# Optimization experiments

Hardware: AMD Instinct MI355X
Metric: run time of the kernel (lower is better)

Reference implementation:

```python
import jax, jax.numpy as jnp
import numpy as np

D = 128
LN_EPS = 1e-5

def _mlp2(x, W1, b1, W2, b2):
    return jax.nn.silu(x @ W1 + b1) @ W2 + b2

def setup_inputs() -> dict:
    key = jax.random.key(0)
    ks = jax.random.split(key, 20)
    B, N = 2, 512
    inp = {
        'scalar_features': jax.random.normal(ks[0], (B, N, D), jnp.float32),
        'vector_features': jax.random.normal(ks[1], (B, N, 3), jnp.float32),
        'positions': jax.random.normal(ks[2], (B, N, 3), jnp.float32),
        'pair_mask': jnp.ones((B, N, N), jnp.float32),
        'conservation': jax.random.uniform(ks[3], (B, N, 1), jnp.float32),
    }
    s = 0.02
    inp['eW1'] = jax.random.normal(ks[4], (2 * D + 4, D), jnp.float32) * s
    inp['eb1'] = jnp.zeros((D,), jnp.float32)
    inp['eW2'] = jax.random.normal(ks[5], (D, D), jnp.float32) * s
    inp['eb2'] = jnp.zeros((D,), jnp.float32)
    inp['sW1'] = jax.random.normal(ks[6], (2 * D, D), jnp.float32) * s
    inp['sb1'] = jnp.zeros((D,), jnp.float32)
    inp['sW2'] = jax.random.normal(ks[7], (D, D), jnp.float32) * s
    inp['sb2'] = jnp.zeros((D,), jnp.float32)
    inp['vW1'] = jax.random.normal(ks[8], (D, D), jnp.float32) * s
    inp['vb1'] = jnp.zeros((D,), jnp.float32)
    inp['vW2'] = jax.random.normal(ks[9], (D, 1), jnp.float32) * s
    inp['vb2'] = jnp.zeros((1,), jnp.float32)
    inp['ln_w'] = jnp.ones((D,), jnp.float32)
    inp['ln_b'] = jnp.zeros((D,), jnp.float32)
    return inp

def reference(scalar_features, vector_features, positions, pair_mask, conservation,
              eW1, eb1, eW2, eb2, sW1, sb1, sW2, sb2, vW1, vb1, vW2, vb2, ln_w, ln_b):
    N = scalar_features.shape[-2]
    # rel[b,i,j] = pos[b,i] - pos[b,j]
    rel = positions[..., :, None, :] - positions[..., None, :, :]          # [B,N,N,3]
    dist = jnp.maximum(jnp.linalg.norm(rel, axis=-1, keepdims=True), 1e-8)  # [B,N,N,1]
    direction = rel / dist
    feat_i = jnp.broadcast_to(scalar_features[..., :, None, :], scalar_features.shape[:-2] + (N, N, D))
    feat_j = jnp.broadcast_to(scalar_features[..., None, :, :], scalar_features.shape[:-2] + (N, N, D))
    cons_i = jnp.broadcast_to(conservation[..., :, None, :], conservation.shape[:-2] + (N, N, 1))
    cons_j = jnp.broadcast_to(conservation[..., None, :, :], conservation.shape[:-2] + (N, N, 1))
    edge_input = jnp.concatenate([feat_i, feat_j, dist, cons_i, cons_j, pair_mask[..., None]], axis=-1)
    edge_hidden = _mlp2(edge_input, eW1, eb1, eW2, eb2)                    # [B,N,N,D]
    edge_weights = jax.nn.sigmoid(edge_hidden.mean(axis=-1)) * pair_mask   # [B,N,N]
    message_scalar = (edge_hidden * edge_weights[..., None]).sum(axis=-2)  # sum over j -> [B,N,D]
    upd = _mlp2(jnp.concatenate([scalar_features, message_scalar], axis=-1), sW1, sb1, sW2, sb2)
    x = scalar_features + upd
    mu = x.mean(axis=-1, keepdims=True)
    var = x.var(axis=-1, keepdims=True)
    scalar_out = (x - mu) * jax.lax.rsqrt(var + LN_EPS) * ln_w + ln_b
    vector_gate = _mlp2(edge_hidden, vW1, vb1, vW2, vb2)[..., 0] * edge_weights  # [B,N,N]
    vector_message = (vector_gate[..., None] * direction).sum(axis=-2)           # [B,N,3]
    vector_out = vector_features + vector_message
    return scalar_out, vector_out, edge_weights
```

## Files before the change

kernel.cpp:

```cpp
#include <hip/hip_runtime.h>

#define DD 128
#define NN 512
#define NODES 1024

typedef short bf16x8 __attribute__((ext_vector_type(8)));
typedef float f32x4 __attribute__((ext_vector_type(4)));

__device__ __forceinline__ float sigmoidf_(float x) {
  return __builtin_amdgcn_rcpf(1.f + __expf(-x));
}
__device__ __forceinline__ float siluf_(float x) { return x * sigmoidf_(x); }

__device__ __forceinline__ unsigned short f2bf_(float v) {
  unsigned int u = __float_as_uint(v);
  u += 0x7fffu + ((u >> 16) & 1u);
  return (unsigned short)(u >> 16);
}
__device__ __forceinline__ unsigned cvtpk_(float lo, float hi) {
  unsigned r;
  asm("v_cvt_pk_bf16_f32 %0, %1, %2" : "=v"(r) : "v"(lo), "v"(hi));
  return r;
}
__device__ __forceinline__ float bflo_(unsigned u) { return __uint_as_float(u << 16); }
__device__ __forceinline__ float bfhi_(unsigned u) { return __uint_as_float(u & 0xffff0000u); }

__global__ __launch_bounds__(128) void prep_kernel(
    const float* __restrict__ sf, const float* __restrict__ cons,
    const float* __restrict__ eW1, const float* __restrict__ eb1,
    const float* __restrict__ eW2, const float* __restrict__ eb2,
    const float* __restrict__ vW1, const float* __restrict__ vb1,
    float* __restrict__ Ag, float* __restrict__ Bvg,
    unsigned short* __restrict__ E2V1T, float* __restrict__ m2,
    float* __restrict__ c1, float* __restrict__ mb)
{
  const int bid = blockIdx.x;
  const int d = threadIdx.x;
  if (bid < NODES) {
    float c = cons[bid];
    float aacc = c * eW1[258*DD + d];
    float bacc = eb1[d] + c * eW1[257*DD + d];
    const float* sfrow = sf + bid*DD;
    #pragma unroll 4
    for (int k = 0; k < DD; ++k) {
      float s = sfrow[k];
      aacc = fmaf(s, eW1[(128+k)*DD + d], aacc);
      bacc = fmaf(s, eW1[k*DD + d], bacc);
    }
    Ag[bid*DD + d]  = aacc;
    Bvg[bid*DD + d] = bacc;
  } else if (bid < NODES + 128) {
    const int k = bid - NODES;
    float acc = 0.f;
    #pragma unroll 4
    for (int t = 0; t < DD; ++t) acc = fmaf(eW2[k*DD + t], vW1[t*DD + d], acc);
    E2V1T[d*DD + (k ^ ((d & 7) << 3))] = f2bf_(acc);
    if (d == 0) {
      float s = 0.f;
      for (int t = 0; t < DD; ++t) s += eW2[k*DD + t];
      m2[k] = s * (1.0f/128.0f);
    }
  } else {
    float acc = vb1[d];
    #pragma unroll 4
    for (int k = 0; k < DD; ++k) acc = fmaf(eb2[k], vW1[k*DD + d], acc);
    c1[d] = acc;
    if (d == 0) {
      float s = 0.f;
      for (int k = 0; k < DD; ++k) s += eb2[k];
      mb[0] = s * (1.0f/128.0f);
    }
  }
}

__global__ __launch_bounds__(256, 2) void edge_kernel(
    const float* __restrict__ sf, const float* __restrict__ vf,
    const float* __restrict__ pos, const float* __restrict__ pm,
    const float* __restrict__ eW1,
    const float* __restrict__ eW2, const float* __restrict__ eb2,
    const float* __restrict__ sW1, const float* __restrict__ sb1,
    const float* __restrict__ sW2, const float* __restrict__ sb2,
    const float* __restrict__ vW2g, const float* __restrict__ vb2g,
    const float* __restrict__ lnw, const float* __restrict__ lnb,
    const float* __restrict__ Ag, const float* __restrict__ Bvg,
    const unsigned short* __restrict__ E2V1Tg, const float* __restrict__ m2g,
    const float* __restrict__ c1g, const float* __restrict__ mbg,
    float* __restrict__ sout, float* __restrict__ vout, float* __restrict__ ewout)
{
  __shared__ __align__(16) unsigned short eTs[128*128];
  __shared__ __align__(16) float BvL[DD], w256L[DD], w259L[DD], m2L[DD];
  __shared__ __align__(16) float c1L[DD], vw2L[DD];
  __shared__ float redS[4], redVx[4], redVy[4], redVz[4], redA[2], redB[2];

  const int tid = threadIdx.x;
  const int ni  = blockIdx.x;
  const int nb  = ni & ~(NN - 1);

  const int l   = tid & 63, w = tid >> 6;
  const int l15 = l & 15,  lg = l >> 4;
  const int d   = tid & 127, sub = tid >> 7;
  const int d0base = lg*8;

  {
    const uint4* src = (const uint4*)E2V1Tg;
    uint4* dst = (uint4*)eTs;
    #pragma unroll
    for (int it = 0; it < 8; ++it) dst[tid + it*256] = src[tid + it*256];
  }
  if (tid < 128) {
    BvL[tid]   = Bvg[(size_t)ni*DD + tid];
    w256L[tid] = eW1[256*DD + tid];
    w259L[tid] = eW1[259*DD + tid];
    m2L[tid]   = m2g[tid];
    c1L[tid]   = c1g[tid];
    vw2L[tid]  = vW2g[tid];
  }
  const float pix = pos[ni*3+0], piy = pos[ni*3+1], piz = pos[ni*3+2];
  const float mbv = mbg[0], vb2v = vb2g[0];

  float Sreg[4][8];
  #pragma unroll
  for (int kk = 0; kk < 4; ++kk)
    #pragma unroll
    for (int m = 0; m < 8; ++m) Sreg[kk][m] = 0.f;
  float vmx = 0.f, vmy = 0.f, vmz = 0.f, swacc = 0.f;

  __syncthreads();

  for (int t = 0; t < 8; ++t) {
    const int row = t*64 + w*16 + l15;
    float px = pos[(nb + row)*3 + 0];
    float py = pos[(nb + row)*3 + 1];
    float pz = pos[(nb + row)*3 + 2];
    float rx = pix - px, ry = piy - py, rz = piz - pz;
    float dist = fmaxf(sqrtf(rx*rx + ry*ry + rz*rz), 1e-8f);
    float inv = __builtin_amdgcn_rcpf(dist);
    float dirx = rx*inv, diry = ry*inv, dirz = rz*inv;
    float mj = pm[(size_t)ni*NN + row];

    uint4 pk0, pk1, pk2, pk3;
    float dot = 0.f;
    const float* agrow = Ag + (size_t)(nb + row)*DD;

#define A_STEP(KK, PK) {                                                        \
    const int d0 = (KK)*32 + d0base;                                            \
    float4 a0 = *(const float4*)(agrow + d0), a1 = *(const float4*)(agrow + d0 + 4); \
    float4 b0 = *(const float4*)&BvL[d0],   b1 = *(const float4*)&BvL[d0+4];    \
    float4 wa0= *(const float4*)&w256L[d0], wa1= *(const float4*)&w256L[d0+4];  \
    float4 wb0= *(const float4*)&w259L[d0], wb1= *(const float4*)&w259L[d0+4];  \
    float4 m20= *(const float4*)&m2L[d0],   m21= *(const float4*)&m2L[d0+4];    \
    float h0 = siluf_(b0.x + a0.x + dist*wa0.x + mj*wb0.x);                     \
    float h1 = siluf_(b0.y + a0.y + dist*wa0.y + mj*wb0.y);                     \
    float h2 = siluf_(b0.z + a0.z + dist*wa0.z + mj*wb0.z);                     \
    float h3 = siluf_(b0.w + a0.w + dist*wa0.w + mj*wb0.w);                     \
    float h4 = siluf_(b1.x + a1.x + dist*wa1.x + mj*wb1.x);                     \
    float h5 = siluf_(b1.y + a1.y + dist*wa1.y + mj*wb1.y);                     \
    float h6 = siluf_(b1.z + a1.z + dist*wa1.z + mj*wb1.z);                     \
    float h7 = siluf_(b1.w + a1.w + dist*wa1.w + mj*wb1.w);                     \
    PK.x = cvtpk_(h0, h1); PK.y = cvtpk_(h2, h3);                               \
    PK.z = cvtpk_(h4, h5); PK.w = cvtpk_(h6, h7);                               \
    dot += h0*m20.x + h1*m20.y + h2*m20.z + h3*m20.w                            \
         + h4*m21.x + h5*m21.y + h6*m21.z + h7*m21.w; }

    A_STEP(0, pk0)
    A_STEP(1, pk1)
    A_STEP(2, pk2)
    A_STEP(3, pk3)
#undef A_STEP

    dot += __shfl_xor(dot, 16);
    dot += __shfl_xor(dot, 32);
    const float w_full = mj * sigmoidf_(dot + mbv);
    if (lg == 0) {
      ewout[(size_t)ni*NN + row] = w_full;
      swacc += w_full;
    }

#define S_STEP(KK, PK) {                                          \
    Sreg[KK][0] = fmaf(w_full, bflo_(PK.x), Sreg[KK][0]);         \
    Sreg[KK][1] = fmaf(w_full, bfhi_(PK.x), Sreg[KK][1]);         \
    Sreg[KK][2] = fmaf(w_full, bflo_(PK.y), Sreg[KK][2]);         \
    Sreg[KK][3] = fmaf(w_full, bfhi_(PK.y), Sreg[KK][3]);         \
    Sreg[KK][4] = fmaf(w_full, bflo_(PK.z), Sreg[KK][4]);         \
    Sreg[KK][5] = fmaf(w_full, bfhi_(PK.z), Sreg[KK][5]);         \
    Sreg[KK][6] = fmaf(w_full, bflo_(PK.w), Sreg[KK][6]);         \
    Sreg[KK][7] = fmaf(w_full, bfhi_(PK.w), Sreg[KK][7]); }

    S_STEP(0, pk0)
    S_STEP(1, pk1)
    S_STEP(2, pk2)
    S_STEP(3, pk3)
#undef S_STEP

    const bf16x8 af0 = __builtin_bit_cast(bf16x8, pk0);
    const bf16x8 af1 = __builtin_bit_cast(bf16x8, pk1);
    const bf16x8 af2 = __builtin_bit_cast(bf16x8, pk2);
    const bf16x8 af3 = __builtin_bit_cast(bf16x8, pk3);

    float gp[4] = {0.f, 0.f, 0.f, 0.f};
    #pragma unroll
    for (int ct = 0; ct < 8; ++ct) {
      const int col = ct*16 + l15;
      const int swz = (col & 7) << 3;
      const unsigned short* ecol = &eTs[col*DD];
      bf16x8 bf0 = *(const bf16x8*)&ecol[(  0 + d0base) ^ swz];
      bf16x8 bf1 = *(const bf16x8*)&ecol[( 32 + d0base) ^ swz];
      bf16x8 bf2 = *(const bf16x8*)&ecol[( 64 + d0base) ^ swz];
      bf16x8 bf3 = *(const bf16x8*)&ecol[( 96 + d0base) ^ swz];
      f32x4 c = {0.f, 0.f, 0.f, 0.f};
      c = __builtin_amdgcn_mfma_f32_16x16x32_bf16(af0, bf0, c, 0, 0, 0);
      c = __builtin_amdgcn_mfma_f32_16x16x32_bf16(af1, bf1, c, 0, 0, 0);
      c = __builtin_amdgcn_mfma_f32_16x16x32_bf16(af2, bf2, c, 0, 0, 0);
      c = __builtin_amdgcn_mfma_f32_16x16x32_bf16(af3, bf3, c, 0, 0, 0);
      const float c1c = c1L[col], vw2c = vw2L[col];
      gp[0] += siluf_(c[0] + c1c) * vw2c;
      gp[1] += siluf_(c[1] + c1c) * vw2c;
      gp[2] += siluf_(c[2] + c1c) * vw2c;
      gp[3] += siluf_(c[3] + c1c) * vw2c;
    }
    #pragma unroll
    for (int r = 0; r < 4; ++r) {
      float v = gp[r];
      v += __shfl_xor(v, 1);
      v += __shfl_xor(v, 2);
      v += __shfl_xor(v, 4);
      v += __shfl_xor(v, 8);
      const int srow = lg*4 + r;
      float wrow = __shfl(w_full, srow);
      float g = (v + vb2v) * wrow;
      float dx = __shfl(dirx, srow);
      float dy = __shfl(diry, srow);
      float dz = __shfl(dirz, srow);
      if (l15 == 0) {
        vmx = fmaf(g, dx, vmx);
        vmy = fmaf(g, dy, vmy);
        vmz = fmaf(g, dz, vmz);
      }
    }
  }

  __syncthreads();
  float* scr   = (float*)eTs;
  float* Spart = scr;
  float* SL    = scr + 512;
  float* partA = scr + 640;
  float* msgL  = scr + 768;
  float* u1L   = scr + 896;
  float* xoL   = scr + 1024;

  #pragma unroll
  for (int kk = 0; kk < 4; ++kk)
    #pragma unroll
    for (int m = 0; m < 8; ++m) {
      float v = Sreg[kk][m];
      v += __shfl_xor(v, 1);
      v += __shfl_xor(v, 2);
      v += __shfl_xor(v, 4);
      v += __shfl_xor(v, 8);
      Sreg[kk][m] = v;
    }
  if (l15 == 0) {
    #pragma unroll
    for (int kk = 0; kk < 4; ++kk)
      #pragma unroll
      for (int m = 0; m < 8; ++m)
        Spart[w*128 + kk*32 + lg*8 + m] = Sreg[kk][m];
  }
  {
    float sw = swacc;
    #pragma unroll
    for (int off = 1; off < 64; off <<= 1) sw += __shfl_xor(sw, off);
    if (l == 0) redS[w] = sw;
  }
  {
    float vx = vmx, vy = vmy, vz = vmz;
    #pragma unroll
    for (int off = 1; off < 64; off <<= 1) {
      vx += __shfl_xor(vx, off);
      vy += __shfl_xor(vy, off);
      vz += __shfl_xor(vz, off);
    }
    if (l == 0) { redVx[w] = vx; redVy[w] = vy; redVz[w] = vz; }
  }
  __syncthreads();
  if (tid < 128) SL[tid] = Spart[tid] + Spart[128+tid] + Spart[256+tid] + Spart[384+tid];
  if (tid == 0) {
    vout[ni*3 + 0] = vf[ni*3 + 0] + redVx[0]+redVx[1]+redVx[2]+redVx[3];
    vout[ni*3 + 1] = vf[ni*3 + 1] + redVy[0]+redVy[1]+redVy[2]+redVy[3];
    vout[ni*3 + 2] = vf[ni*3 + 2] + redVz[0]+redVz[1]+redVz[2]+redVz[3];
  }
  __syncthreads();
  const float sumwv = redS[0] + redS[1] + redS[2] + redS[3];

  float p = 0.f;
  { int k0 = sub*64;
    #pragma unroll 4
    for (int k = k0; k < k0 + 64; ++k) p = fmaf(SL[k], eW2[k*DD + d], p); }
  if (sub) partA[d] = p;
  __syncthreads();
  if (!sub) msgL[d] = p + partA[d] + sumwv * eb2[d];
  __syncthreads();

  float q = 0.f;
  if (!sub) {
    const float* xr = sf + (size_t)ni*DD;
    #pragma unroll 4
    for (int tt = 0; tt < 128; ++tt) q = fmaf(xr[tt], sW1[tt*DD + d], q);
  } else {
    #pragma unroll 4
    for (int tt = 0; tt < 128; ++tt) q = fmaf(msgL[tt], sW1[(128 + tt)*DD + d], q);
  }
  if (sub) partA[d] = q;
  __syncthreads();
  if (!sub) u1L[d] = siluf_(q + partA[d] + sb1[d]);
  __syncthreads();

  float r2 = 0.f;
  { int t0 = sub*64;
    #pragma unroll 4
    for (int tt = t0; tt < t0 + 64; ++tt) r2 = fmaf(u1L[tt], sW2[tt*DD + d], r2); }
  if (sub) partA[d] = r2;
  __syncthreads();
  if (!sub) xoL[d] = sf[(size_t)ni*DD + d] + r2 + partA[d] + sb2[d];
  __syncthreads();

  if (tid < 128) {
    float v = xoL[tid];
    float s1 = v, s2 = v*v;
    #pragma unroll
    for (int off = 1; off < 64; off <<= 1) { s1 += __shfl_xor(s1, off); s2 += __shfl_xor(s2, off); }
    if ((tid & 63) == 0) { redA[tid >> 6] = s1; redB[tid >> 6] = s2; }
  }
  __syncthreads();
  if (tid < 128) {
    float s1 = redA[0] + redA[1], s2 = redB[0] + redB[1];
    float mu = s1 * 0.0078125f;
    float var = s2 * 0.0078125f - mu*mu;
    sout[(size_t)ni*DD + tid] = (xoL[tid] - mu) * rsqrtf(var + 1e-5f) * lnw[tid] + lnb[tid];
  }
}

extern "C" void kernel_launch(void* const* d_in, const int* in_sizes, int n_in,
                              void* d_out, int out_size, void* d_ws, size_t ws_size,
                              hipStream_t stream) {
  const float* sf   = (const float*)d_in[0];
  const float* vf   = (const float*)d_in[1];
  const float* pos  = (const float*)d_in[2];
  const float* pm   = (const float*)d_in[3];
  const float* cons = (const float*)d_in[4];
  const float* eW1  = (const float*)d_in[5];
  const float* eb1  = (const float*)d_in[6];
  const float* eW2  = (const float*)d_in[7];
  const float* eb2  = (const float*)d_in[8];
  const float* sW1  = (const float*)d_in[9];
  const float* sb1  = (const float*)d_in[10];
  const float* sW2  = (const float*)d_in[11];
  const float* sb2  = (const float*)d_in[12];
  const float* vW1  = (const float*)d_in[13];
  const float* vb1  = (const float*)d_in[14];
  const float* vW2  = (const float*)d_in[15];
  const float* vb2  = (const float*)d_in[16];
  const float* lnw  = (const float*)d_in[17];
  const float* lnb  = (const float*)d_in[18];

  float* ws   = (float*)d_ws;
  float* Ag   = ws;
  float* Bvg  = ws + 131072;
  float* m2   = ws + 262144;
  float* c1   = ws + 262272;
  float* mb   = ws + 262400;
  unsigned short* E2V1T = (unsigned short*)(ws + 262404);

  float* sout  = (float*)d_out;
  float* vout  = sout + 131072;
  float* ewout = sout + 134144;

  hipLaunchKernelGGL(prep_kernel, dim3(NODES + 129), dim3(128), 0, stream,
                     sf, cons, eW1, eb1, eW2, eb2, vW1, vb1,
                     Ag, Bvg, E2V1T, m2, c1, mb);
  hipLaunchKernelGGL(edge_kernel, dim3(NODES), dim3(256), 0, stream,
                     sf, vf, pos, pm, eW1, eW2, eb2, sW1, sb1, sW2, sb2,
                     vW2, vb2, lnw, lnb, Ag, Bvg, E2V1T, m2, c1, mb,
                     sout, vout, ewout);
}
```

Measured before the change: 103.5 us.

## Read fused weight matrix from global/L2 instead of staging in LDS, raise occupancy

```diff
diff --git a/kernel.cpp b/kernel.cpp
--- a/kernel.cpp
+++ b/kernel.cpp
@@ -54,7 +54,7 @@
     float acc = 0.f;
     #pragma unroll 4
     for (int t = 0; t < DD; ++t) acc = fmaf(eW2[k*DD + t], vW1[t*DD + d], acc);
-    E2V1T[d*DD + (k ^ ((d & 7) << 3))] = f2bf_(acc);
+    E2V1T[d*DD + k] = f2bf_(acc);
     if (d == 0) {
       float s = 0.f;
       for (int t = 0; t < DD; ++t) s += eW2[k*DD + t];
@@ -73,7 +73,7 @@
   }
 }
 
-__global__ __launch_bounds__(256, 2) void edge_kernel(
+__global__ __launch_bounds__(256, 4) void edge_kernel(
     const float* __restrict__ sf, const float* __restrict__ vf,
     const float* __restrict__ pos, const float* __restrict__ pm,
     const float* __restrict__ eW1,
@@ -87,9 +87,9 @@
     const float* __restrict__ c1g, const float* __restrict__ mbg,
     float* __restrict__ sout, float* __restrict__ vout, float* __restrict__ ewout)
 {
-  __shared__ __align__(16) unsigned short eTs[128*128];
   __shared__ __align__(16) float BvL[DD], w256L[DD], w259L[DD], m2L[DD];
   __shared__ __align__(16) float c1L[DD], vw2L[DD];
+  __shared__ __align__(16) float scr2[1152];
   __shared__ float redS[4], redVx[4], redVy[4], redVz[4], redA[2], redB[2];
 
   const int tid = threadIdx.x;
@@ -101,12 +101,6 @@
   const int d   = tid & 127, sub = tid >> 7;
   const int d0base = lg*8;
 
-  {
-    const uint4* src = (const uint4*)E2V1Tg;
-    uint4* dst = (uint4*)eTs;
-    #pragma unroll
-    for (int it = 0; it < 8; ++it) dst[tid + it*256] = src[tid + it*256];
-  }
   if (tid < 128) {
     BvL[tid]   = Bvg[(size_t)ni*DD + tid];
     w256L[tid] = eW1[256*DD + tid];
@@ -201,12 +195,11 @@
     #pragma unroll
     for (int ct = 0; ct < 8; ++ct) {
       const int col = ct*16 + l15;
-      const int swz = (col & 7) << 3;
-      const unsigned short* ecol = &eTs[col*DD];
-      bf16x8 bf0 = *(const bf16x8*)&ecol[(  0 + d0base) ^ swz];
-      bf16x8 bf1 = *(const bf16x8*)&ecol[( 32 + d0base) ^ swz];
-      bf16x8 bf2 = *(const bf16x8*)&ecol[( 64 + d0base) ^ swz];
-      bf16x8 bf3 = *(const bf16x8*)&ecol[( 96 + d0base) ^ swz];
+      const unsigned short* ecol = E2V1Tg + (size_t)col*DD + d0base;
+      bf16x8 bf0 = *(const bf16x8*)(ecol);
+      bf16x8 bf1 = *(const bf16x8*)(ecol + 32);
+      bf16x8 bf2 = *(const bf16x8*)(ecol + 64);
+      bf16x8 bf3 = *(const bf16x8*)(ecol + 96);
       f32x4 c = {0.f, 0.f, 0.f, 0.f};
       c = __builtin_amdgcn_mfma_f32_16x16x32_bf16(af0, bf0, c, 0, 0, 0);
       c = __builtin_amdgcn_mfma_f32_16x16x32_bf16(af1, bf1, c, 0, 0, 0);
@@ -239,14 +232,12 @@
     }
   }
 
-  __syncthreads();
-  float* scr   = (float*)eTs;
-  float* Spart = scr;
-  float* SL    = scr + 512;
-  float* partA = scr + 640;
-  float* msgL  = scr + 768;
-  float* u1L   = scr + 896;
-  float* xoL   = scr + 1024;
+  float* Spart = scr2;
+  float* SL    = scr2 + 512;
+  float* partA = scr2 + 640;
+  float* msgL  = scr2 + 768;
+  float* u1L   = scr2 + 896;
+  float* xoL   = scr2 + 1024;
 
   #pragma unroll
   for (int kk = 0; kk < 4; ++kk)
```

Result: slower. 243.9 us (+135.6%).

## Process two edge rows per iteration and split node-MLP dot-product accumulators

Applied to the files above, without the earlier changes.

```diff
diff --git a/kernel.cpp b/kernel.cpp
--- a/kernel.cpp
+++ b/kernel.cpp
@@ -90,6 +90,7 @@
   __shared__ __align__(16) unsigned short eTs[128*128];
   __shared__ __align__(16) float BvL[DD], w256L[DD], w259L[DD], m2L[DD];
   __shared__ __align__(16) float c1L[DD], vw2L[DD];
+  __shared__ __align__(16) float scr2[1152];
   __shared__ float redS[4], redVx[4], redVy[4], redVz[4], redA[2], redB[2];
 
   const int tid = threadIdx.x;
@@ -127,77 +128,105 @@
 
   __syncthreads();
 
-  for (int t = 0; t < 8; ++t) {
-    const int row = t*64 + w*16 + l15;
-    float px = pos[(nb + row)*3 + 0];
-    float py = pos[(nb + row)*3 + 1];
-    float pz = pos[(nb + row)*3 + 2];
-    float rx = pix - px, ry = piy - py, rz = piz - pz;
-    float dist = fmaxf(sqrtf(rx*rx + ry*ry + rz*rz), 1e-8f);
-    float inv = __builtin_amdgcn_rcpf(dist);
-    float dirx = rx*inv, diry = ry*inv, dirz = rz*inv;
-    float mj = pm[(size_t)ni*NN + row];
-
-    uint4 pk0, pk1, pk2, pk3;
-    float dot = 0.f;
-    const float* agrow = Ag + (size_t)(nb + row)*DD;
-
-#define A_STEP(KK, PK) {                                                        \
-    const int d0 = (KK)*32 + d0base;                                            \
-    float4 a0 = *(const float4*)(agrow + d0), a1 = *(const float4*)(agrow + d0 + 4); \
-    float4 b0 = *(const float4*)&BvL[d0],   b1 = *(const float4*)&BvL[d0+4];    \
-    float4 wa0= *(const float4*)&w256L[d0], wa1= *(const float4*)&w256L[d0+4];  \
-    float4 wb0= *(const float4*)&w259L[d0], wb1= *(const float4*)&w259L[d0+4];  \
-    float4 m20= *(const float4*)&m2L[d0],   m21= *(const float4*)&m2L[d0+4];    \
-    float h0 = siluf_(b0.x + a0.x + dist*wa0.x + mj*wb0.x);                     \
-    float h1 = siluf_(b0.y + a0.y + dist*wa0.y + mj*wb0.y);                     \
-    float h2 = siluf_(b0.z + a0.z + dist*wa0.z + mj*wb0.z);                     \
-    float h3 = siluf_(b0.w + a0.w + dist*wa0.w + mj*wb0.w);                     \
-    float h4 = siluf_(b1.x + a1.x + dist*wa1.x + mj*wb1.x);                     \
-    float h5 = siluf_(b1.y + a1.y + dist*wa1.y + mj*wb1.y);                     \
-    float h6 = siluf_(b1.z + a1.z + dist*wa1.z + mj*wb1.z);                     \
-    float h7 = siluf_(b1.w + a1.w + dist*wa1.w + mj*wb1.w);                     \
-    PK.x = cvtpk_(h0, h1); PK.y = cvtpk_(h2, h3);                               \
-    PK.z = cvtpk_(h4, h5); PK.w = cvtpk_(h6, h7);                               \
-    dot += h0*m20.x + h1*m20.y + h2*m20.z + h3*m20.w                            \
-         + h4*m21.x + h5*m21.y + h6*m21.z + h7*m21.w; }
-
-    A_STEP(0, pk0)
-    A_STEP(1, pk1)
-    A_STEP(2, pk2)
-    A_STEP(3, pk3)
-#undef A_STEP
-
-    dot += __shfl_xor(dot, 16);
-    dot += __shfl_xor(dot, 32);
-    const float w_full = mj * sigmoidf_(dot + mbv);
+  for (int t = 0; t < 4; ++t) {
+    const int row0 = t*128 + w*16 + l15;
+    const int row1 = row0 + 64;
+    float p0x = pos[(nb + row0)*3 + 0], p0y = pos[(nb + row0)*3 + 1], p0z = pos[(nb + row0)*3 + 2];
+    float p1x = pos[(nb + row1)*3 + 0], p1y = pos[(nb + row1)*3 + 1], p1z = pos[(nb + row1)*3 + 2];
+    float r0x = pix - p0x, r0y = piy - p0y, r0z = piz - p0z;
+    float r1x = pix - p1x, r1y = piy - p1y, r1z = piz - p1z;
+    float dist0 = fmaxf(sqrtf(r0x*r0x + r0y*r0y + r0z*r0z), 1e-8f);
+    float dist1 = fmaxf(sqrtf(r1x*r1x + r1y*r1y + r1z*r1z), 1e-8f);
+    float inv0 = __builtin_amdgcn_rcpf(dist0);
+    float inv1 = __builtin_amdgcn_rcpf(dist1);
+    float dir0x = r0x*inv0, dir0y = r0y*inv0, dir0z = r0z*inv0;
+    float dir1x = r1x*inv1, dir1y = r1y*inv1, dir1z = r1z*inv1;
+    float mj0 = pm[(size_t)ni*NN + row0];
+    float mj1 = pm[(size_t)ni*NN + row1];
+
+    uint4 pkA0, pkA1, pkA2, pkA3, pkB0, pkB1, pkB2, pkB3;
+    float dot0 = 0.f, dot1 = 0.f;
+    const float* ag0 = Ag + (size_t)(nb + row0)*DD;
+    const float* ag1 = Ag + (size_t)(nb + row1)*DD;
+
+#define A_STEP2(KK, PKA, PKB) {                                                   \
+    const int d0 = (KK)*32 + d0base;                                              \
+    float4 b0 = *(const float4*)&BvL[d0],   b1 = *(const float4*)&BvL[d0+4];      \
+    float4 wa0= *(const float4*)&w256L[d0], wa1= *(const float4*)&w256L[d0+4];    \
+    float4 wb0= *(const float4*)&w259L[d0], wb1= *(const float4*)&w259L[d0+4];    \
+    float4 m20= *(const float4*)&m2L[d0],   m21= *(const float4*)&m2L[d0+4];      \
+    float4 aa0 = *(const float4*)(ag0 + d0), aa1 = *(const float4*)(ag0 + d0 + 4);\
+    float4 ba0 = *(const float4*)(ag1 + d0), ba1 = *(const float4*)(ag1 + d0 + 4);\
+    float u0 = siluf_(b0.x + aa0.x + dist0*wa0.x + mj0*wb0.x);                    \
+    float u1 = siluf_(b0.y + aa0.y + dist0*wa0.y + mj0*wb0.y);                    \
+    float u2 = siluf_(b0.z + aa0.z + dist0*wa0.z + mj0*wb0.z);                    \
+    float u3 = siluf_(b0.w + aa0.w + dist0*wa0.w + mj0*wb0.w);                    \
+    float u4 = siluf_(b1.x + aa1.x + dist0*wa1.x + mj0*wb1.x);                    \
+    float u5 = siluf_(b1.y + aa1.y + dist0*wa1.y + mj0*wb1.y);                    \
+    float u6 = siluf_(b1.z + aa1.z + dist0*wa1.z + mj0*wb1.z);                    \
+    float u7 = siluf_(b1.w + aa1.w + dist0*wa1.w + mj0*wb1.w);                    \
+    float v0 = siluf_(b0.x + ba0.x + dist1*wa0.x + mj1*wb0.x);                    \
+    float v1 = siluf_(b0.y + ba0.y + dist1*wa0.y + mj1*wb0.y);                    \
+    float v2 = siluf_(b0.z + ba0.z + dist1*wa0.z + mj1*wb0.z);                    \
+    float v3 = siluf_(b0.w + ba0.w + dist1*wa0.w + mj1*wb0.w);                    \
+    float v4 = siluf_(b1.x + ba1.x + dist1*wa1.x + mj1*wb1.x);                    \
+    float v5 = siluf_(b1.y + ba1.y + dist1*wa1.y + mj1*wb1.y);                    \
+    float v6 = siluf_(b1.z + ba1.z + dist1*wa1.z + mj1*wb1.z);                    \
+    float v7 = siluf_(b1.w + ba1.w + dist1*wa1.w + mj1*wb1.w);                    \
+    PKA.x = cvtpk_(u0,u1); PKA.y = cvtpk_(u2,u3);                                 \
+    PKA.z = cvtpk_(u4,u5); PKA.w = cvtpk_(u6,u7);                                 \
+    PKB.x = cvtpk_(v0,v1); PKB.y = cvtpk_(v2,v3);                                 \
+    PKB.z = cvtpk_(v4,v5); PKB.w = cvtpk_(v6,v7);                                 \
+    dot0 += u0*m20.x + u1*m20.y + u2*m20.z + u3*m20.w                             \
+          + u4*m21.x + u5*m21.y + u6*m21.z + u7*m21.w;                            \
+    dot1 += v0*m20.x + v1*m20.y + v2*m20.z + v3*m20.w                             \
+          + v4*m21.x + v5*m21.y + v6*m21.z + v7*m21.w; }
+
+    A_STEP2(0, pkA0, pkB0)
+    A_STEP2(1, pkA1, pkB1)
+    A_STEP2(2, pkA2, pkB2)
+    A_STEP2(3, pkA3, pkB3)
+#undef A_STEP2
+
+    dot0 += __shfl_xor(dot0, 16);
+    dot0 += __shfl_xor(dot0, 32);
+    dot1 += __shfl_xor(dot1, 16);
+    dot1 += __shfl_xor(dot1, 32);
+    const float w0 = mj0 * sigmoidf_(dot0 + mbv);
+    const float w1 = mj1 * sigmoidf_(dot1 + mbv);
     if (lg == 0) {
-      ewout[(size_t)ni*NN + row] = w_full;
-      swacc += w_full;
-    }
-
-#define S_STEP(KK, PK) {                                          \
-    Sreg[KK][0] = fmaf(w_full, bflo_(PK.x), Sreg[KK][0]);         \
-    Sreg[KK][1] = fmaf(w_full, bfhi_(PK.x), Sreg[KK][1]);         \
-    Sreg[KK][2] = fmaf(w_full, bflo_(PK.y), Sreg[KK][2]);         \
-    Sreg[KK][3] = fmaf(w_full, bfhi_(PK.y), Sreg[KK][3]);         \
-    Sreg[KK][4] = fmaf(w_full, bflo_(PK.z), Sreg[KK][4]);         \
-    Sreg[KK][5] = fmaf(w_full, bfhi_(PK.z), Sreg[KK][5]);         \
-    Sreg[KK][6] = fmaf(w_full, bflo_(PK.w), Sreg[KK][6]);         \
-    Sreg[KK][7] = fmaf(w_full, bfhi_(PK.w), Sreg[KK][7]); }
-
-    S_STEP(0, pk0)
-    S_STEP(1, pk1)
-    S_STEP(2, pk2)
-    S_STEP(3, pk3)
-#undef S_STEP
-
-    const bf16x8 af0 = __builtin_bit_cast(bf16x8, pk0);
-    const bf16x8 af1 = __builtin_bit_cast(bf16x8, pk1);
-    const bf16x8 af2 = __builtin_bit_cast(bf16x8, pk2);
-    const bf16x8 af3 = __builtin_bit_cast(bf16x8, pk3);
-
-    float gp[4] = {0.f, 0.f, 0.f, 0.f};
+      ewout[(size_t)ni*NN + row0] = w0;
+      ewout[(size_t)ni*NN + row1] = w1;
+      swacc += w0 + w1;
+    }
+
+#define S_STEP2(KK, PKA, PKB) {                                                       \
+    Sreg[KK][0] = fmaf(w1, bflo_(PKB.x), fmaf(w0, bflo_(PKA.x), Sreg[KK][0]));        \
+    Sreg[KK][1] = fmaf(w1, bfhi_(PKB.x), fmaf(w0, bfhi_(PKA.x), Sreg[KK][1]));        \
+    Sreg[KK][2] = fmaf(w1, bflo_(PKB.y), fmaf(w0, bflo_(PKA.y), Sreg[KK][2]));        \
+    Sreg[KK][3] = fmaf(w1, bfhi_(PKB.y), fmaf(w0, bfhi_(PKA.y), Sreg[KK][3]));        \
+    Sreg[KK][4] = fmaf(w1, bflo_(PKB.z), fmaf(w0, bflo_(PKA.z), Sreg[KK][4]));        \
+    Sreg[KK][5] = fmaf(w1, bfhi_(PKB.z), fmaf(w0, bfhi_(PKA.z), Sreg[KK][5]));        \
+    Sreg[KK][6] = fmaf(w1, bflo_(PKB.w), fmaf(w0, bflo_(PKA.w), Sreg[KK][6]));        \
+    Sreg[KK][7] = fmaf(w1, bfhi_(PKB.w), fmaf(w0, bfhi_(PKA.w), Sreg[KK][7])); }
+
+    S_STEP2(0, pkA0, pkB0)
+    S_STEP2(1, pkA1, pkB1)
+    S_STEP2(2, pkA2, pkB2)
+    S_STEP2(3, pkA3, pkB3)
+#undef S_STEP2
+
+    const bf16x8 afA0 = __builtin_bit_cast(bf16x8, pkA0);
+    const bf16x8 afA1 = __builtin_bit_cast(bf16x8, pkA1);
+    const bf16x8 afA2 = __builtin_bit_cast(bf16x8, pkA2);
+    const bf16x8 afA3 = __builtin_bit_cast(bf16x8, pkA3);
+    const bf16x8 afB0 = __builtin_bit_cast(bf16x8, pkB0);
+    const bf16x8 afB1 = __builtin_bit_cast(bf16x8, pkB1);
+    const bf16x8 afB2 = __builtin_bit_cast(bf16x8, pkB2);
+    const bf16x8 afB3 = __builtin_bit_cast(bf16x8, pkB3);
+
+    float gp0[4] = {0.f,0.f,0.f,0.f};
+    float gp1[4] = {0.f,0.f,0.f,0.f};
     #pragma unroll
     for (int ct = 0; ct < 8; ++ct) {
       const int col = ct*16 + l15;
@@ -207,46 +236,54 @@
       bf16x8 bf1 = *(const bf16x8*)&ecol[( 32 + d0base) ^ swz];
       bf16x8 bf2 = *(const bf16x8*)&ecol[( 64 + d0base) ^ swz];
       bf16x8 bf3 = *(const bf16x8*)&ecol[( 96 + d0base) ^ swz];
-      f32x4 c = {0.f, 0.f, 0.f, 0.f};
-      c = __builtin_amdgcn_mfma_f32_16x16x32_bf16(af0, bf0, c, 0, 0, 0);
-      c = __builtin_amdgcn_mfma_f32_16x16x32_bf16(af1, bf1, c, 0, 0, 0);
-      c = __builtin_amdgcn_mfma_f32_16x16x32_bf16(af2, bf2, c, 0, 0, 0);
-      c = __builtin_amdgcn_mfma_f32_16x16x32_bf16(af3, bf3, c, 0, 0, 0);
+      f32x4 c0 = {0.f,0.f,0.f,0.f};
+      f32x4 c1v = {0.f,0.f,0.f,0.f};
+      c0  = __builtin_amdgcn_mfma_f32_16x16x32_bf16(afA0, bf0, c0, 0, 0, 0);
+      c1v = __builtin_amdgcn_mfma_f32_16x16x32_bf16(afB0, bf0, c1v, 0, 0, 0);
+      c0  = __builtin_amdgcn_mfma_f32_16x16x32_bf16(afA1, bf1, c0, 0, 0, 0);
+      c1v = __builtin_amdgcn_mfma_f32_16x16x32_bf16(afB1, bf1, c1v, 0, 0, 0);
+      c0  = __builtin_amdgcn_mfma_f32_16x16x32_bf16(afA2, bf2, c0, 0, 0, 0);
+      c1v = __builtin_amdgcn_mfma_f32_16x16x32_bf16(afB2, bf2, c1v, 0, 0, 0);
+      c0  = __builtin_amdgcn_mfma_f32_16x16x32_bf16(afA3, bf3, c0, 0, 0, 0);
+      c1v = __builtin_amdgcn_mfma_f32_16x16x32_bf16(afB3, bf3, c1v, 0, 0, 0);
       const float c1c = c1L[col], vw2c = vw2L[col];
-      gp[0] += siluf_(c[0] + c1c) * vw2c;
-      gp[1] += siluf_(c[1] + c1c) * vw2c;
-      gp[2] += siluf_(c[2] + c1c) * vw2c;
-      gp[3] += siluf_(c[3] + c1c) * vw2c;
+      gp0[0] += siluf_(c0[0]  + c1c) * vw2c;
+      gp0[1] += siluf_(c0[1]  + c1c) * vw2c;
+      gp0[2] += siluf_(c0[2]  + c1c) * vw2c;
+      gp0[3] += siluf_(c0[3]  + c1c) * vw2c;
+      gp1[0] += siluf_(c1v[0] + c1c) * vw2c;
+      gp1[1] += siluf_(c1v[1] + c1c) * vw2c;
+      gp1[2] += siluf_(c1v[2] + c1c) * vw2c;
+      gp1[3] += siluf_(c1v[3] + c1c) * vw2c;
     }
     #pragma unroll
     for (int r = 0; r < 4; ++r) {
-      float v = gp[r];
-      v += __shfl_xor(v, 1);
-      v += __shfl_xor(v, 2);
-      v += __shfl_xor(v, 4);
-      v += __shfl_xor(v, 8);
+      float v0 = gp0[r], v1 = gp1[r];
+      v0 += __shfl_xor(v0, 1);  v1 += __shfl_xor(v1, 1);
+      v0 += __shfl_xor(v0, 2);  v1 += __shfl_xor(v1, 2);
+      v0 += __shfl_xor(v0, 4);  v1 += __shfl_xor(v1, 4);
+      v0 += __shfl_xor(v0, 8);  v1 += __shfl_xor(v1, 8);
       const int srow = lg*4 + r;
-      float wrow = __shfl(w_full, srow);
-      float g = (v + vb2v) * wrow;
-      float dx = __shfl(dirx, srow);
-      float dy = __shfl(diry, srow);
-      float dz = __shfl(dirz, srow);
+      float wr0 = __shfl(w0, srow);
+      float wr1 = __shfl(w1, srow);
+      float g0 = (v0 + vb2v) * wr0;
+      float g1 = (v1 + vb2v) * wr1;
+      float d0x = __shfl(dir0x, srow), d0y = __shfl(dir0y, srow), d0z = __shfl(dir0z, srow);
+      float d1x = __shfl(dir1x, srow), d1y = __shfl(dir1y, srow), d1z = __shfl(dir1z, srow);
       if (l15 == 0) {
-        vmx = fmaf(g, dx, vmx);
-        vmy = fmaf(g, dy, vmy);
-        vmz = fmaf(g, dz, vmz);
+        vmx = fmaf(g0, d0x, fmaf(g1, d1x, vmx));
+        vmy = fmaf(g0, d0y, fmaf(g1, d1y, vmy));
+        vmz = fmaf(g0, d0z, fmaf(g1, d1z, vmz));
       }
     }
   }
 
-  __syncthreads();
-  float* scr   = (float*)eTs;
-  float* Spart = scr;
-  float* SL    = scr + 512;
-  float* partA = scr + 640;
-  float* msgL  = scr + 768;
-  float* u1L   = scr + 896;
-  float* xoL   = scr + 1024;
+  float* Spart = scr2;
+  float* SL    = scr2 + 512;
+  float* partA = scr2 + 640;
+  float* msgL  = scr2 + 768;
+  float* u1L   = scr2 + 896;
+  float* xoL   = scr2 + 1024;
 
   #pragma unroll
   for (int kk = 0; kk < 4; ++kk)
@@ -294,8 +331,13 @@
 
   float p = 0.f;
   { int k0 = sub*64;
-    #pragma unroll 4
-    for (int k = k0; k < k0 + 64; ++k) p = fmaf(SL[k], eW2[k*DD + d], p); }
+    float pa = 0.f, pb = 0.f;
+    #pragma unroll 4
+    for (int k = k0; k < k0 + 32; ++k) {
+      pa = fmaf(SL[k], eW2[k*DD + d], pa);
+      pb = fmaf(SL[k+32], eW2[(k+32)*DD + d], pb);
+    }
+    p = pa + pb; }
   if (sub) partA[d] = p;
   __syncthreads();
   if (!sub) msgL[d] = p + partA[d] + sumwv * eb2[d];
@@ -304,11 +346,21 @@
   float q = 0.f;
   if (!sub) {
     const float* xr = sf + (size_t)ni*DD;
-    #pragma unroll 4
-    for (int tt = 0; tt < 128; ++tt) q = fmaf(xr[tt], sW1[tt*DD + d], q);
+    float qa = 0.f, qb = 0.f;
+    #pragma unroll 4
+    for (int tt = 0; tt < 64; ++tt) {
+      qa = fmaf(xr[tt], sW1[tt*DD + d], qa);
+      qb = fmaf(xr[tt+64], sW1[(tt+64)*DD + d], qb);
+    }
+    q = qa + qb;
   } else {
-    #pragma unroll 4
-    for (int tt = 0; tt < 128; ++tt) q = fmaf(msgL[tt], sW1[(128 + tt)*DD + d], q);
+    float qa = 0.f, qb = 0.f;
+    #pragma unroll 4
+    for (int tt = 0; tt < 64; ++tt) {
+      qa = fmaf(msgL[tt], sW1[(128 + tt)*DD + d], qa);
+      qb = fmaf(msgL[tt+64], sW1[(192 + tt)*DD + d], qb);
+    }
+    q = qa + qb;
   }
   if (sub) partA[d] = q;
   __syncthreads();
@@ -317,8 +369,13 @@
 
   float r2 = 0.f;
   { int t0 = sub*64;
-    #pragma unroll 4
-    for (int tt = t0; tt < t0 + 64; ++tt) r2 = fmaf(u1L[tt], sW2[tt*DD + d], r2); }
+    float ra = 0.f, rb = 0.f;
+    #pragma unroll 4
+    for (int tt = t0; tt < t0 + 32; ++tt) {
+      ra = fmaf(u1L[tt], sW2[tt*DD + d], ra);
+      rb = fmaf(u1L[tt+32], sW2[(tt+32)*DD + d], rb);
+    }
+    r2 = ra + rb; }
   if (sub) partA[d] = r2;
   __syncthreads();
   if (!sub) xoL[d] = sf[(size_t)ni*DD + d] + r2 + partA[d] + sb2[d];
```

Result: faster. 95.43 us (-7.8%).
